# Kernel tuning notes

Hardware: AMD Instinct MI355X
Metric: run time of the kernel (lower is better)

Reference implementation:

```python
import jax, jax.numpy as jnp
import numpy as np

F0_DIM, PH_DIM, MIDI_DIM, DUR_DIM = 64, 128, 64, 64
COND = 256
TOTAL = F0_DIM + PH_DIM + MIDI_DIM + DUR_DIM  # 320
EPS = 1e-5


def setup_inputs() -> dict:
    key = jax.random.key(0)
    ks = jax.random.split(key, 16)
    B, T = 16, 4096
    inp = {
        "f0": jax.random.uniform(ks[0], (B, T), jnp.float32) * 400.0 + 80.0,
        "phone": jax.random.randint(ks[1], (B, T), 0, 100, jnp.int32),
        "duration": jax.random.uniform(ks[2], (B, T), jnp.float32),
        "midi": jax.random.randint(ks[3], (B, T), 0, 128, jnp.int32),
        # f0 encoder: Linear(1,32) -> ReLU -> Linear(32,64)
        "f0_w1": jax.random.normal(ks[4], (1, F0_DIM // 2), jnp.float32) * 0.1,
        "f0_b1": jnp.zeros((F0_DIM // 2,), jnp.float32),
        "f0_w2": jax.random.normal(ks[5], (F0_DIM // 2, F0_DIM), jnp.float32) * 0.1,
        "f0_b2": jnp.zeros((F0_DIM,), jnp.float32),
        # embeddings
        "phone_table": jax.random.normal(ks[6], (100, PH_DIM), jnp.float32),
        "midi_table": jax.random.normal(ks[7], (128, MIDI_DIM), jnp.float32),
        # duration encoder: Linear(1,32) -> ReLU -> Linear(32,64)
        "dur_w1": jax.random.normal(ks[8], (1, DUR_DIM // 2), jnp.float32) * 0.1,
        "dur_b1": jnp.zeros((DUR_DIM // 2,), jnp.float32),
        "dur_w2": jax.random.normal(ks[9], (DUR_DIM // 2, DUR_DIM), jnp.float32) * 0.1,
        "dur_b2": jnp.zeros((DUR_DIM,), jnp.float32),
        # projection: Linear(320,256) -> LayerNorm(256) -> ReLU -> Linear(256,256)
        "proj_w1": jax.random.normal(ks[10], (TOTAL, COND), jnp.float32) * (1.0 / np.sqrt(TOTAL)),
        "proj_b1": jnp.zeros((COND,), jnp.float32),
        "ln_g": jnp.ones((COND,), jnp.float32),
        "ln_b": jnp.zeros((COND,), jnp.float32),
        "proj_w2": jax.random.normal(ks[11], (COND, COND), jnp.float32) * (1.0 / np.sqrt(COND)),
        "proj_b2": jnp.zeros((COND,), jnp.float32),
    }
    return inp


def reference(f0, phone, duration, midi,
              f0_w1, f0_b1, f0_w2, f0_b2,
              phone_table, midi_table,
              dur_w1, dur_b1, dur_w2, dur_b2,
              proj_w1, proj_b1, ln_g, ln_b, proj_w2, proj_b2):
    # f0 / duration MLPs, vectorized over all (batch, time) positions
    f0_h = jax.nn.relu(f0[..., None] * f0_w1[0] + f0_b1)            # [B,T,32]
    f0_emb = f0_h @ f0_w2 + f0_b2                                    # [B,T,64]
    dur_h = jax.nn.relu(duration[..., None] * dur_w1[0] + dur_b1)    # [B,T,32]
    dur_emb = dur_h @ dur_w2 + dur_b2                                # [B,T,64]
    phone_emb = phone_table[phone]                                   # [B,T,128]
    midi_emb = midi_table[midi]                                      # [B,T,64]
    combined = jnp.concatenate([f0_emb, phone_emb, midi_emb, dur_emb], axis=-1)  # [B,T,320]
    h = combined @ proj_w1 + proj_b1                                 # [B,T,256]
    mu = jnp.mean(h, axis=-1, keepdims=True)
    var = jnp.mean((h - mu) ** 2, axis=-1, keepdims=True)
    h = (h - mu) * jax.lax.rsqrt(var + EPS) * ln_g + ln_b
    h = jax.nn.relu(h)
    return h @ proj_w2 + proj_b2                                     # [B,T,256]
```

## Files before the change

kernel.cpp:

```cpp
#include <hip/hip_runtime.h>

typedef _Float16 f16x8 __attribute__((ext_vector_type(8)));
typedef float f32x4 __attribute__((ext_vector_type(4)));
typedef unsigned int u32x2 __attribute__((ext_vector_type(2)));

#define MROWS 65536
#define BM 128
#define NBLK (MROWS / BM)

#define B1F_OFF 0u
#define B2F_OFF 65536u
#define TP_OFF 196608u
#define TM_OFF 299008u
#define BC_OFF 430080u
#define WFD_OFF 431104u


__device__ __forceinline__ unsigned a2off(unsigned X) {
  return (X * 16u) ^ (X & 0x30u);
}

__global__ __launch_bounds__(256) void prep_tables(
    const float* __restrict__ f0_w2, const float* __restrict__ f0_b2,
    const float* __restrict__ ptab, const float* __restrict__ mtab,
    const float* __restrict__ dur_w2, const float* __restrict__ dur_b2,
    const float* __restrict__ W1, const float* __restrict__ pb1,
    float* __restrict__ wsf) {
  const int r = blockIdx.x, n = threadIdx.x;
  if (r < 64) {
    float s = 0.f;
    if (r < 32) {
      for (int j = 0; j < 64; ++j) s = fmaf(f0_w2[r * 64 + j], W1[j * 256 + n], s);
    } else {
      for (int j = 0; j < 64; ++j) s = fmaf(dur_w2[(r - 32) * 64 + j], W1[(256 + j) * 256 + n], s);
    }
    wsf[WFD_OFF / 4 + r * 256 + n] = s;
  } else if (r < 164) {
    const int p = r - 64;
    float s = 0.f;
    for (int j = 0; j < 128; ++j) s = fmaf(ptab[p * 128 + j], W1[(64 + j) * 256 + n], s);
    wsf[TP_OFF / 4 + p * 256 + n] = s;
  } else if (r < 292) {
    const int m = r - 164;
    float s = 0.f;
    for (int j = 0; j < 64; ++j) s = fmaf(mtab[m * 64 + j], W1[(192 + j) * 256 + n], s);
    wsf[TM_OFF / 4 + m * 256 + n] = s;
  } else {
    float s = pb1[n];
    for (int j = 0; j < 64; ++j) {
      s = fmaf(f0_b2[j], W1[j * 256 + n], s);
      s = fmaf(dur_b2[j], W1[(256 + j) * 256 + n], s);
    }
    wsf[BC_OFF / 4 + n] = s;
  }
}

__global__ __launch_bounds__(64) void prep_frags(const float* __restrict__ W2, char* __restrict__ ws) {
  const float* Wfd = (const float*)(ws + WFD_OFF);
  const int t = blockIdx.x;
  const int l = threadIdx.x;
  const int qq = l >> 4, c = l & 15;
  if (t < 32) {
    const int kt = t >> 4, nt = t & 15;
    const int col = (nt >> 2) * 64 + c * 4 + (nt & 3);
    f16x8 v;
#pragma unroll
    for (int e = 0; e < 8; ++e) {
      const int k = kt * 32 + 4 * qq + (e & 3) + 16 * (e >> 2);
      v[e] = (_Float16)Wfd[k * 256 + col];
    }
    *(f16x8*)(ws + B1F_OFF + (unsigned)((kt * 16 + nt) * 64 + l) * 16u) = v;
  } else {
    const int t2 = t - 32;
    const int kt = t2 >> 4, nt = t2 & 15;
    const int col = (nt >> 2) * 64 + c * 4 + (nt & 3);
    f16x8 v;
#pragma unroll
    for (int e = 0; e < 8; ++e) {
      const int k = kt * 32 + 4 * qq + (e & 3) + 16 * (e >> 2);
      v[e] = (_Float16)W2[k * 256 + col];
    }
    *(f16x8*)(ws + B2F_OFF + (unsigned)((kt * 16 + nt) * 64 + l) * 16u) = v;
  }
}

__global__ __launch_bounds__(256, 2) void cond_enc_main(
    const float* __restrict__ f0g, const int* __restrict__ phone,
    const float* __restrict__ durg, const int* __restrict__ midi,
    const float* __restrict__ f0_w1, const float* __restrict__ f0_b1,
    const float* __restrict__ dur_w1, const float* __restrict__ dur_b1,
    const float* __restrict__ ln_g, const float* __restrict__ ln_b,
    const float* __restrict__ pb2, const char* __restrict__ ws,
    float* __restrict__ out) {
  __shared__ __align__(16) unsigned char smem[4 * 16384];

  const int tid = threadIdx.x;
  const int l = tid & 63;
  const int w = tid >> 6;
  const int q = l >> 4;
  const int c = l & 15;
  const int rowbase = blockIdx.x * BM + w * 32;
  unsigned char* Asc = smem + w * 16384;

  const float* Tp = (const float*)(ws + TP_OFF);
  const float* Tm = (const float*)(ws + TM_OFF);

  const int rl = l & 31;
  const float xf_all = f0g[rowbase + rl];
  const float xd_all = durg[rowbase + rl];
  const int ph_all = phone[rowbase + rl];
  const int md_all = midi[rowbase + rl];

  f16x8 a1[2][2];
#pragma unroll
  for (int i = 0; i < 2; ++i) {
    const float xf = __shfl(xf_all, i * 16 + c);
    const float xd = __shfl(xd_all, i * 16 + c);
#pragma unroll
    for (int kh = 0; kh < 2; ++kh) {
      f16x8 v;
#pragma unroll
      for (int e = 0; e < 8; ++e) {
        const int ki = 4 * q + (e & 3) + 16 * (e >> 2);
        const float wv = kh ? dur_w1[ki] : f0_w1[ki];
        const float bv = kh ? dur_b1[ki] : f0_b1[ki];
        const float x = kh ? xd : xf;
        v[e] = (_Float16)fmaxf(fmaf(x, wv, bv), 0.f);
      }
      a1[i][kh] = v;
    }
  }

  const f32x4 zero4 = {0.f, 0.f, 0.f, 0.f};
  f32x4 acc[2][16];
#pragma unroll
  for (int i = 0; i < 2; ++i)
#pragma unroll
    for (int nt = 0; nt < 16; ++nt) acc[i][nt] = zero4;
  {
    const f16x8* B1p = (const f16x8*)(ws + B1F_OFF);
#pragma unroll
    for (int kt = 0; kt < 2; ++kt) {
      f16x8 bfr[16];
#pragma unroll
      for (int nt = 0; nt < 16; ++nt) bfr[nt] = B1p[(kt * 16 + nt) * 64 + l];
#pragma unroll
      for (int i = 0; i < 2; ++i)
#pragma unroll
        for (int nt = 0; nt < 16; ++nt)
          acc[i][nt] = __builtin_amdgcn_mfma_f32_16x16x32_f16(a1[i][kt], bfr[nt], acc[i][nt], 0, 0, 0);
    }
  }

  const float* bcp = (const float*)(ws + BC_OFF);
  f32x4 bc4[4], g4[4], lb4[4];
#pragma unroll
  for (int g = 0; g < 4; ++g) {
    bc4[g] = *(const f32x4*)(bcp + g * 64 + c * 4);
    g4[g] = *(const f32x4*)(ln_g + g * 64 + c * 4);
    lb4[g] = *(const f32x4*)(ln_b + g * 64 + c * 4);
  }
  const int lp_base = 16 * (c & 3);
  const unsigned hoff = (unsigned)((c >> 2) & 1) * 8u;
#pragma unroll
  for (int i = 0; i < 2; ++i) {
#pragma unroll
    for (int r = 0; r < 4; ++r) {
      const int rrel = i * 16 + q * 4 + r;
      const int ph = __shfl(ph_all, rrel);
      const int md = __shfl(md_all, rrel);
      f32x4 tp4[4], tm4[4];
#pragma unroll
      for (int g = 0; g < 4; ++g) {
        tp4[g] = *(const f32x4*)(Tp + ph * 256 + g * 64 + c * 4);
        tm4[g] = *(const f32x4*)(Tm + md * 256 + g * 64 + c * 4);
      }
      float s = 0.f, ss = 0.f;
#pragma unroll
      for (int nt = 0; nt < 16; ++nt) {
        const int g = nt >> 2, bq = nt & 3;
        float v = acc[i][nt][r] + bc4[g][bq] + tp4[g][bq] + tm4[g][bq];
        acc[i][nt][r] = v;
        s += v;
        ss = fmaf(v, v, ss);
      }
#pragma unroll
      for (int m = 1; m < 16; m <<= 1) {
        s += __shfl_xor(s, m, 64);
        ss += __shfl_xor(ss, m, 64);
      }
      const float mu = s * (1.f / 256.f);
      const float var = fmaxf(ss * (1.f / 256.f) - mu * mu, 0.f);
      const float rstd = rsqrtf(var + 1e-5f);
#pragma unroll
      for (int g = 0; g < 4; ++g) {
        unsigned short hw[4];
#pragma unroll
        for (int bq = 0; bq < 4; ++bq) {
          float v = fmaf((acc[i][4 * g + bq][r] - mu) * rstd, g4[g][bq], lb4[g][bq]);
          v = fmaxf(v, 0.f);
          hw[bq] = __builtin_bit_cast(unsigned short, (_Float16)v);
        }
        u32x2 pkt;
        pkt[0] = (unsigned)hw[0] | ((unsigned)hw[1] << 16);
        pkt[1] = (unsigned)hw[2] | ((unsigned)hw[3] << 16);
        const int kt = 2 * g + (c >> 3);
        const unsigned X = (unsigned)((kt * 2 + i) * 64 + (q * 4 + r + lp_base));
        *(u32x2*)(Asc + a2off(X) + hoff) = pkt;
      }
    }
  }

#pragma unroll
  for (int i = 0; i < 2; ++i)
#pragma unroll
    for (int nt = 0; nt < 16; ++nt) acc[i][nt] = zero4;
  {
    const f16x8* B2p = (const f16x8*)(ws + B2F_OFF);
#pragma unroll
    for (int kt = 0; kt < 8; ++kt) {
      f16x8 a0 = *(const f16x8*)(Asc + a2off((unsigned)((kt * 2 + 0) * 64 + l)));
      f16x8 a1f = *(const f16x8*)(Asc + a2off((unsigned)((kt * 2 + 1) * 64 + l)));
      f16x8 bfr[16];
#pragma unroll
      for (int nt = 0; nt < 16; ++nt) bfr[nt] = B2p[(kt * 16 + nt) * 64 + l];
#pragma unroll
      for (int nt = 0; nt < 16; ++nt) {
        acc[0][nt] = __builtin_amdgcn_mfma_f32_16x16x32_f16(a0, bfr[nt], acc[0][nt], 0, 0, 0);
        acc[1][nt] = __builtin_amdgcn_mfma_f32_16x16x32_f16(a1f, bfr[nt], acc[1][nt], 0, 0, 0);
      }
    }
  }

  f32x4 b24[4];
#pragma unroll
  for (int g = 0; g < 4; ++g) b24[g] = *(const f32x4*)(pb2 + g * 64 + c * 4);
#pragma unroll
  for (int i = 0; i < 2; ++i)
#pragma unroll
    for (int r = 0; r < 4; ++r) {
      const int grow = rowbase + i * 16 + q * 4 + r;
#pragma unroll
      for (int g = 0; g < 4; ++g) {
        f32x4 st;
#pragma unroll
        for (int bq = 0; bq < 4; ++bq) st[bq] = acc[i][4 * g + bq][r] + b24[g][bq];
        __builtin_nontemporal_store(st, (f32x4*)(out + grow * 256 + g * 64 + c * 4));
      }
    }
}

extern "C" void kernel_launch(void* const* d_in, const int* in_sizes, int n_in,
                              void* d_out, int out_size, void* d_ws, size_t ws_size,
                              hipStream_t stream) {
  (void)in_sizes; (void)n_in; (void)out_size; (void)ws_size;
  const float* f0 = (const float*)d_in[0];
  const int* phone = (const int*)d_in[1];
  const float* dur = (const float*)d_in[2];
  const int* midi = (const int*)d_in[3];
  const float* f0_w1 = (const float*)d_in[4];
  const float* f0_b1 = (const float*)d_in[5];
  const float* f0_w2 = (const float*)d_in[6];
  const float* f0_b2 = (const float*)d_in[7];
  const float* ptab = (const float*)d_in[8];
  const float* mtab = (const float*)d_in[9];
  const float* dur_w1 = (const float*)d_in[10];
  const float* dur_b1 = (const float*)d_in[11];
  const float* dur_w2 = (const float*)d_in[12];
  const float* dur_b2 = (const float*)d_in[13];
  const float* W1 = (const float*)d_in[14];
  const float* pb1 = (const float*)d_in[15];
  const float* ln_g = (const float*)d_in[16];
  const float* ln_b = (const float*)d_in[17];
  const float* W2 = (const float*)d_in[18];
  const float* pb2 = (const float*)d_in[19];
  char* ws = (char*)d_ws;
  float* out = (float*)d_out;

  prep_tables<<<293, 256, 0, stream>>>(f0_w2, f0_b2, ptab, mtab, dur_w2, dur_b2, W1, pb1, (float*)ws);
  prep_frags<<<160, 64, 0, stream>>>(W2, ws);
  cond_enc_main<<<NBLK, 256, 0, stream>>>(f0, phone, dur, midi, f0_w1, f0_b1, dur_w1, dur_b1,
                                          ln_g, ln_b, pb2, ws, out);
}
```

Baseline: 39.24 us.

## Split output columns across two waves sharing each 32-row tile

```diff
diff --git a/kernel.cpp b/kernel.cpp
--- a/kernel.cpp
+++ b/kernel.cpp
@@ -5,7 +5,7 @@
 typedef unsigned int u32x2 __attribute__((ext_vector_type(2)));
 
 #define MROWS 65536
-#define BM 128
+#define BM 32
 #define NBLK (MROWS / BM)
 
 #define B1F_OFF 0u
@@ -84,7 +84,7 @@
   }
 }
 
-__global__ __launch_bounds__(256, 2) void cond_enc_main(
+__global__ __launch_bounds__(128, 4) void cond_enc_main(
     const float* __restrict__ f0g, const int* __restrict__ phone,
     const float* __restrict__ durg, const int* __restrict__ midi,
     const float* __restrict__ f0_w1, const float* __restrict__ f0_b1,
@@ -92,15 +92,16 @@
     const float* __restrict__ ln_g, const float* __restrict__ ln_b,
     const float* __restrict__ pb2, const char* __restrict__ ws,
     float* __restrict__ out) {
-  __shared__ __align__(16) unsigned char smem[4 * 16384];
+  __shared__ __align__(16) unsigned char smem[16384 + 512];
+  unsigned char* Pbuf = smem;
+  float* partials = (float*)(smem + 16384);
 
   const int tid = threadIdx.x;
   const int l = tid & 63;
-  const int w = tid >> 6;
+  const int wc = tid >> 6;
   const int q = l >> 4;
   const int c = l & 15;
-  const int rowbase = blockIdx.x * BM + w * 32;
-  unsigned char* Asc = smem + w * 16384;
+  const int rowbase = blockIdx.x * BM;
 
   const float* Tp = (const float*)(ws + TP_OFF);
   const float* Tm = (const float*)(ws + TM_OFF);
@@ -132,36 +133,35 @@
   }
 
   const f32x4 zero4 = {0.f, 0.f, 0.f, 0.f};
-  f32x4 acc[2][16];
+  f32x4 acc[2][8];
 #pragma unroll
   for (int i = 0; i < 2; ++i)
 #pragma unroll
-    for (int nt = 0; nt < 16; ++nt) acc[i][nt] = zero4;
+    for (int j = 0; j < 8; ++j) acc[i][j] = zero4;
   {
     const f16x8* B1p = (const f16x8*)(ws + B1F_OFF);
 #pragma unroll
     for (int kt = 0; kt < 2; ++kt) {
-      f16x8 bfr[16];
-#pragma unroll
-      for (int nt = 0; nt < 16; ++nt) bfr[nt] = B1p[(kt * 16 + nt) * 64 + l];
+      f16x8 bfr[8];
+#pragma unroll
+      for (int j = 0; j < 8; ++j) bfr[j] = B1p[(kt * 16 + wc * 8 + j) * 64 + l];
 #pragma unroll
       for (int i = 0; i < 2; ++i)
 #pragma unroll
-        for (int nt = 0; nt < 16; ++nt)
-          acc[i][nt] = __builtin_amdgcn_mfma_f32_16x16x32_f16(a1[i][kt], bfr[nt], acc[i][nt], 0, 0, 0);
+        for (int j = 0; j < 8; ++j)
+          acc[i][j] = __builtin_amdgcn_mfma_f32_16x16x32_f16(a1[i][kt], bfr[j], acc[i][j], 0, 0, 0);
     }
   }
 
   const float* bcp = (const float*)(ws + BC_OFF);
-  f32x4 bc4[4], g4[4], lb4[4];
-#pragma unroll
-  for (int g = 0; g < 4; ++g) {
-    bc4[g] = *(const f32x4*)(bcp + g * 64 + c * 4);
-    g4[g] = *(const f32x4*)(ln_g + g * 64 + c * 4);
-    lb4[g] = *(const f32x4*)(ln_b + g * 64 + c * 4);
-  }
-  const int lp_base = 16 * (c & 3);
-  const unsigned hoff = (unsigned)((c >> 2) & 1) * 8u;
+  f32x4 bc4[2], g4[2], lb4[2];
+#pragma unroll
+  for (int gl = 0; gl < 2; ++gl) {
+    const int g = wc * 2 + gl;
+    bc4[gl] = *(const f32x4*)(bcp + g * 64 + c * 4);
+    g4[gl] = *(const f32x4*)(ln_g + g * 64 + c * 4);
+    lb4[gl] = *(const f32x4*)(ln_b + g * 64 + c * 4);
+  }
 #pragma unroll
   for (int i = 0; i < 2; ++i) {
 #pragma unroll
@@ -169,18 +169,19 @@
       const int rrel = i * 16 + q * 4 + r;
       const int ph = __shfl(ph_all, rrel);
       const int md = __shfl(md_all, rrel);
-      f32x4 tp4[4], tm4[4];
-#pragma unroll
-      for (int g = 0; g < 4; ++g) {
-        tp4[g] = *(const f32x4*)(Tp + ph * 256 + g * 64 + c * 4);
-        tm4[g] = *(const f32x4*)(Tm + md * 256 + g * 64 + c * 4);
+      f32x4 tp4[2], tm4[2];
+#pragma unroll
+      for (int gl = 0; gl < 2; ++gl) {
+        const int g = wc * 2 + gl;
+        tp4[gl] = *(const f32x4*)(Tp + ph * 256 + g * 64 + c * 4);
+        tm4[gl] = *(const f32x4*)(Tm + md * 256 + g * 64 + c * 4);
       }
       float s = 0.f, ss = 0.f;
 #pragma unroll
-      for (int nt = 0; nt < 16; ++nt) {
-        const int g = nt >> 2, bq = nt & 3;
-        float v = acc[i][nt][r] + bc4[g][bq] + tp4[g][bq] + tm4[g][bq];
-        acc[i][nt][r] = v;
+      for (int j = 0; j < 8; ++j) {
+        const int gl = j >> 2, bq = j & 3;
+        float v = acc[i][j][r] + bc4[gl][bq] + tp4[gl][bq] + tm4[gl][bq];
+        acc[i][j][r] = v;
         s += v;
         ss = fmaf(v, v, ss);
       }
@@ -189,15 +190,34 @@
         s += __shfl_xor(s, m, 64);
         ss += __shfl_xor(ss, m, 64);
       }
+      if (c == 0) {
+        partials[rrel * 4 + wc * 2 + 0] = s;
+        partials[rrel * 4 + wc * 2 + 1] = ss;
+      }
+    }
+  }
+  __syncthreads();
+
+  const int lp_base = 16 * (c & 3);
+  const unsigned hoff = (unsigned)((c >> 2) & 1) * 8u;
+#pragma unroll
+  for (int i = 0; i < 2; ++i) {
+#pragma unroll
+    for (int r = 0; r < 4; ++r) {
+      const int rrel = i * 16 + q * 4 + r;
+      const f32x4 pr = *(const f32x4*)(partials + rrel * 4);
+      const float s = pr[0] + pr[2];
+      const float ss = pr[1] + pr[3];
       const float mu = s * (1.f / 256.f);
       const float var = fmaxf(ss * (1.f / 256.f) - mu * mu, 0.f);
       const float rstd = rsqrtf(var + 1e-5f);
 #pragma unroll
-      for (int g = 0; g < 4; ++g) {
+      for (int gl = 0; gl < 2; ++gl) {
+        const int g = wc * 2 + gl;
         unsigned short hw[4];
 #pragma unroll
         for (int bq = 0; bq < 4; ++bq) {
-          float v = fmaf((acc[i][4 * g + bq][r] - mu) * rstd, g4[g][bq], lb4[g][bq]);
+          float v = fmaf((acc[i][4 * gl + bq][r] - mu) * rstd, g4[gl][bq], lb4[gl][bq]);
           v = fmaxf(v, 0.f);
           hw[bq] = __builtin_bit_cast(unsigned short, (_Float16)v);
         }
@@ -206,45 +226,47 @@
         pkt[1] = (unsigned)hw[2] | ((unsigned)hw[3] << 16);
         const int kt = 2 * g + (c >> 3);
         const unsigned X = (unsigned)((kt * 2 + i) * 64 + (q * 4 + r + lp_base));
-        *(u32x2*)(Asc + a2off(X) + hoff) = pkt;
-      }
-    }
-  }
+        *(u32x2*)(Pbuf + a2off(X) + hoff) = pkt;
+      }
+    }
+  }
+  __syncthreads();
 
 #pragma unroll
   for (int i = 0; i < 2; ++i)
 #pragma unroll
-    for (int nt = 0; nt < 16; ++nt) acc[i][nt] = zero4;
+    for (int j = 0; j < 8; ++j) acc[i][j] = zero4;
   {
     const f16x8* B2p = (const f16x8*)(ws + B2F_OFF);
 #pragma unroll
     for (int kt = 0; kt < 8; ++kt) {
-      f16x8 a0 = *(const f16x8*)(Asc + a2off((unsigned)((kt * 2 + 0) * 64 + l)));
-      f16x8 a1f = *(const f16x8*)(Asc + a2off((unsigned)((kt * 2 + 1) * 64 + l)));
-      f16x8 bfr[16];
-#pragma unroll
-      for (int nt = 0; nt < 16; ++nt) bfr[nt] = B2p[(kt * 16 + nt) * 64 + l];
-#pragma unroll
-      for (int nt = 0; nt < 16; ++nt) {
-        acc[0][nt] = __builtin_amdgcn_mfma_f32_16x16x32_f16(a0, bfr[nt], acc[0][nt], 0, 0, 0);
-        acc[1][nt] = __builtin_amdgcn_mfma_f32_16x16x32_f16(a1f, bfr[nt], acc[1][nt], 0, 0, 0);
-      }
-    }
-  }
-
-  f32x4 b24[4];
-#pragma unroll
-  for (int g = 0; g < 4; ++g) b24[g] = *(const f32x4*)(pb2 + g * 64 + c * 4);
+      const f16x8 a0 = *(const f16x8*)(Pbuf + a2off((unsigned)((kt * 2 + 0) * 64 + l)));
+      const f16x8 a1f = *(const f16x8*)(Pbuf + a2off((unsigned)((kt * 2 + 1) * 64 + l)));
+      f16x8 bfr[8];
+#pragma unroll
+      for (int j = 0; j < 8; ++j) bfr[j] = B2p[(kt * 16 + wc * 8 + j) * 64 + l];
+#pragma unroll
+      for (int j = 0; j < 8; ++j) {
+        acc[0][j] = __builtin_amdgcn_mfma_f32_16x16x32_f16(a0, bfr[j], acc[0][j], 0, 0, 0);
+        acc[1][j] = __builtin_amdgcn_mfma_f32_16x16x32_f16(a1f, bfr[j], acc[1][j], 0, 0, 0);
+      }
+    }
+  }
+
+  f32x4 b24[2];
+#pragma unroll
+  for (int gl = 0; gl < 2; ++gl) b24[gl] = *(const f32x4*)(pb2 + (wc * 2 + gl) * 64 + c * 4);
 #pragma unroll
   for (int i = 0; i < 2; ++i)
 #pragma unroll
     for (int r = 0; r < 4; ++r) {
       const int grow = rowbase + i * 16 + q * 4 + r;
 #pragma unroll
-      for (int g = 0; g < 4; ++g) {
+      for (int gl = 0; gl < 2; ++gl) {
+        const int g = wc * 2 + gl;
         f32x4 st;
 #pragma unroll
-        for (int bq = 0; bq < 4; ++bq) st[bq] = acc[i][4 * g + bq][r] + b24[g][bq];
+        for (int bq = 0; bq < 4; ++bq) st[bq] = acc[i][4 * gl + bq][r] + b24[gl][bq];
         __builtin_nontemporal_store(st, (f32x4*)(out + grow * 256 + g * 64 + c * 4));
       }
     }
@@ -279,6 +301,6 @@
 
   prep_tables<<<293, 256, 0, stream>>>(f0_w2, f0_b2, ptab, mtab, dur_w2, dur_b2, W1, pb1, (float*)ws);
   prep_frags<<<160, 64, 0, stream>>>(W2, ws);
-  cond_enc_main<<<NBLK, 256, 0, stream>>>(f0, phone, dur, midi, f0_w1, f0_b1, dur_w1, dur_b1,
+  cond_enc_main<<<NBLK, 128, 0, stream>>>(f0, phone, dur, midi, f0_w1, f0_b1, dur_w1, dur_b1,
                                           ln_g, ln_b, pb2, ws, out);
 }
```

After: 52.46 us. 1.34x slower.
